# Kernel optimization log

Measured on AMD Instinct MI355X. Metric: run time of the kernel, lower is better.

Reference implementation:

```python
import jax, jax.numpy as jnp
import numpy as np

N_REL = 8


def setup_inputs() -> dict:
    key = jax.random.key(0)
    ks = jax.random.split(key, 16)
    N, E = 100_000, 1_600_000
    rn = lambda k, shape, s=0.1: jax.random.normal(k, shape, dtype=jnp.float32) * s
    return {
        "x": rn(ks[0], (N, 3), 1.0),
        "edge_index": jax.random.randint(ks[1], (2, E), 0, N),
        "edge_attr": rn(ks[2], (E, 2), 1.0),
        "edge_type": jax.random.randint(ks[3], (E,), 0, N_REL),
        "omega": rn(ks[4], (N, 2), 1.0),
        # encoder weights
        "Wn": rn(ks[5], (3, 64)), "bn": jnp.zeros((64,), jnp.float32),
        "We": rn(ks[6], (2, 32)), "be": jnp.zeros((32,), jnp.float32),
        "Wo": rn(ks[7], (2, 64)), "bo": jnp.zeros((64,), jnp.float32),
        # RGCN layer 1 (edge-feature-aware): per-relation W over concat(x_src, e) -> 64
        "W1": rn(ks[8], (N_REL, 96, 64)), "Wroot1": rn(ks[9], (64, 64)), "b1": jnp.zeros((64,), jnp.float32),
        # RGCN layer 2 (PyG RGCNConv, aggr='max')
        "W2": rn(ks[10], (N_REL, 64, 64)), "Wroot2": rn(ks[11], (64, 64)), "b2": jnp.zeros((64,), jnp.float32),
        # head
        "Wagg": rn(ks[12], (128, 64)), "bagg": jnp.zeros((64,), jnp.float32),
        "Wc": rn(ks[13], (64, 1)), "bc": jnp.zeros((1,), jnp.float32),
    }


def reference(x, edge_index, edge_attr, edge_type, omega,
              Wn, bn, We, be, Wo, bo,
              W1, Wroot1, b1, W2, Wroot2, b2,
              Wagg, bagg, Wc, bc):
    N = x.shape[0]
    n = jax.nn.relu(x @ Wn + bn)            # [N,64]
    e = jax.nn.relu(edge_attr @ We + be)    # [E,32]
    o = jax.nn.relu(omega @ Wo + bo)        # [N,64]
    src, dst = edge_index[0], edge_index[1]

    # --- RGCN layer 1: per-relation transform of [x_src || e], sum-aggregate ---
    feat = jnp.concatenate([n[src], e], axis=1)  # [E,96]
    acc = n @ Wroot1 + b1                        # root/self term
    for r in range(N_REL):
        m = (edge_type == r).astype(feat.dtype)[:, None]
        acc = acc + jax.ops.segment_sum((feat * m) @ W1[r], dst, num_segments=N)
    h = jax.nn.relu(acc)                         # [N,64]

    # --- RGCN layer 2: per-relation transform of x_src, max-aggregate per relation, sum over relations ---
    hs = h[src]                                  # [E,64]
    neg = jnp.finfo(h.dtype).min
    acc2 = h @ Wroot2 + b2
    for r in range(N_REL):
        mask = (edge_type == r)[:, None]
        msg = jnp.where(mask, hs @ W2[r], neg)
        mx = jax.ops.segment_max(msg, dst, num_segments=N)
        acc2 = acc2 + jnp.where(mx > neg * 0.5, mx, 0.0)  # empty segments -> 0 (PyG zeros-init scatter)
    h2 = jax.nn.relu(acc2)                       # [N,64]

    out = jax.nn.relu(jnp.concatenate([h2, o], axis=1) @ Wagg + bagg)
    return jnp.tanh(out @ Wc + bc) * 5.0
```

## Files before the change

### kernel.cpp

```cpp
#include <hip/hip_runtime.h>
#include <cmath>

typedef __attribute__((ext_vector_type(8))) short short8;
typedef __attribute__((ext_vector_type(4))) float floatx4;

__device__ __forceinline__ unsigned short rnbf(float f) {
    unsigned u = __float_as_uint(f);
    u += 0x7fffu + ((u >> 16) & 1u);
    return (unsigned short)(u >> 16);
}
__device__ __forceinline__ float bf2f(unsigned short h) {
    return __uint_as_float(((unsigned)h) << 16);
}
__device__ __forceinline__ int rfl(int v) { return __builtin_amdgcn_readfirstlane(v); }
__device__ __forceinline__ float eAct(unsigned ry, float we0, float we1, float bev) {
    float a0 = __uint_as_float(ry & 0xFFFF0000u);
    float a1 = __uint_as_float(ry << 16);
    return fmaxf(fmaf(a1, we1, fmaf(a0, we0, bev)), 0.f);
}
__device__ __forceinline__ unsigned vidx(int x, unsigned pl, int lane) {
    return (((unsigned)x >> 24) & 7u)*pl + (unsigned)(x & 0xFFFFFF)*64u + (unsigned)lane;
}
__device__ __forceinline__ void mstep(int r, float v, int& cur, float& mx, float& add) {
    bool nb = (r != cur);
    add += nb ? mx : 0.f;
    mx = nb ? v : fmaxf(mx, v);
    cur = r;
}

__global__ void k_histd(const int* __restrict__ ei, const int* __restrict__ et,
                        int* __restrict__ deg8, int E)
{
    int e = blockIdx.x*blockDim.x + threadIdx.x;
    if (e < E) atomicAdd(&deg8[ei[E + e]*8 + et[e]], 1);
}
#define SCHUNK 1024
__global__ void k_bsum(const int* __restrict__ deg, int* __restrict__ bsum, int K)
{
    __shared__ int s[256];
    int b = blockIdx.x, t = threadIdx.x;
    int base = b*SCHUNK;
    int v = 0;
    for (int k = t; k < SCHUNK; k += 256) { int i = base + k; v += (i < K) ? deg[i] : 0; }
    s[t] = v; __syncthreads();
    for (int o = 128; o; o >>= 1) { if (t < o) s[t] += s[t+o]; __syncthreads(); }
    if (t == 0) bsum[b] = s[0];
}
__global__ void k_bscan(int* __restrict__ bsum, int nb)
{
    __shared__ int ts[256];
// ... 57 lines not shown
}

#define PB_KEYS 4096
#define PA_CH   4096
#define CNTB    512

__device__ __forceinline__ void dev_cnt(const int* __restrict__ ei,
                                        int* __restrict__ bktCnt,
                                        int E, int nbkt, int cb, int cgrid)
{
    __shared__ int cnt[512];
    for (int j = threadIdx.x; j < nbkt; j += 256) cnt[j] = 0;
    __syncthreads();
    int stride = cgrid*256;
    for (int e = cb*256 + threadIdx.x; e < E; e += stride)
        atomicAdd(&cnt[ei[E + e] >> 9], 1);
    __syncthreads();
    for (int j = threadIdx.x; j < nbkt; j += 256) {
        int c = cnt[j];
        if (c) atomicAdd(&bktCnt[j], c);
    }
}

__device__ __forceinline__ void dev_encV(
    const float* __restrict__ x,
    const float* __restrict__ Wn, const float* __restrict__ bn,
    const unsigned short* __restrict__ wpk, const float* __restrict__ b1,
    float* __restrict__ acc1, unsigned short* __restrict__ Vbf,
    size_t plane, int N, int bid)
{
    int lane = threadIdx.x & 63;
    int wave = threadIdx.x >> 6;
    int n0 = bid*64 + 16*wave;
    int m = lane & 15, q = lane >> 4;
    int node = n0 + m; if (node >= N) node = N - 1;
    float x0 = x[3*node], x1 = x[3*node+1], x2 = x[3*node+2];
    short8 ah[2], al[2];
    #pragma unroll
    for (int ks = 0; ks < 2; ++ks) {
        #pragma unroll
        for (int i = 0; i < 8; ++i) {
            int f = ks*32 + q*8 + i;
            float nf = fmaxf(fmaf(x2, Wn[128+f], fmaf(x1, Wn[64+f], fmaf(x0, Wn[f], bn[f]))), 0.f);
            unsigned short hb = rnbf(nf);
            ah[ks][i] = (short)hb;
            al[ks][i] = (short)rnbf(nf - bf2f(hb));
        }
    }
    {
        floatx4 acc[4];
        #pragma unroll
        for (int jt = 0; jt < 4; ++jt) acc[jt] = (floatx4){0.f,0.f,0.f,0.f};
        #pragma unroll
        for (int ks = 0; ks < 2; ++ks) {
            int unit = 40 + ks;
            #pragma unroll
            for (int jt = 0; jt < 4; ++jt) {
                const unsigned short* qp = wpk + (((size_t)unit*4 + jt)*64 + lane)*16;
                short8 bh = *(const short8*)qp;
                short8 bl = *(const short8*)(qp + 8);
                acc[jt] = __builtin_amdgcn_mfma_f32_16x16x32_bf16(ah[ks], bh, acc[jt], 0,0,0);
                acc[jt] = __builtin_amdgcn_mfma_f32_16x16x32_bf16(ah[ks], bl, acc[jt], 0,0,0);
                acc[jt] = __builtin_amdgcn_mfma_f32_16x16x32_bf16(al[ks], bh, acc[jt], 0,0,0);
            }
        }
        #pragma unroll
        for (int jt = 0; jt < 4; ++jt) {
            float bb = b1[jt*16 + m];
            #pragma unroll
            for (int t = 0; t < 4; ++t) {
                int row = n0 + q*4 + t;
                if (row < N) acc1[(size_t)row*64 + jt*16 + m] = acc[jt][t] + bb;
            }
        }
    }
    for (int p = 0; p < 8; ++p) {
        floatx4 acc[4];
        #pragma unroll
        for (int jt = 0; jt < 4; ++jt) acc[jt] = (floatx4){0.f,0.f,0.f,0.f};
        #pragma unroll
        for (int ks = 0; ks < 2; ++ks) {
            int unit = p*2 + ks;
            #pragma unroll
            for (int jt = 0; jt < 4; ++jt) {
                const unsigned short* qp = wpk + (((size_t)unit*4 + jt)*64 + lane)*16;
                short8 bh = *(const short8*)qp;
                short8 bl = *(const short8*)(qp + 8);
                acc[jt] = __builtin_amdgcn_mfma_f32_16x16x32_bf16(ah[ks], bh, acc[jt], 0,0,0);
                acc[jt] = __builtin_amdgcn_mfma_f32_16x16x32_bf16(ah[ks], bl, acc[jt], 0,0,0);
                acc[jt] = __builtin_amdgcn_mfma_f32_16x16x32_bf16(al[ks], bh, acc[jt], 0,0,0);
            }
        }
        unsigned short* Vp = Vbf + (size_t)p*plane;
        #pragma unroll
        for (int jt = 0; jt < 4; ++jt) {
            #pragma unroll
            for (int t = 0; t < 4; ++t) {
                int row = n0 + q*4 + t;
                if (row < N) Vp[(size_t)row*64 + jt*16 + m] = rnbf(acc[jt][t]);
            }
        }
    }
}

__global__ __launch_bounds__(256) void k_phase1(
    const float* __restrict__ x,
    const float* __restrict__ Wn, const float* __restrict__ bn,
    const unsigned short* __restrict__ wpk, const float* __restrict__ b1,
    float* __restrict__ acc1, unsigned short* __restrict__ Vbf,
    size_t plane, int N,
    const int* __restrict__ ei, int* __restrict__ bktCnt, int E, int nbkt,
    int encBlocks, int cntBlocks)
{
    int bid = (int)blockIdx.x;
    if (bid < encBlocks) {
        dev_encV(x, Wn, bn, wpk, b1, acc1, Vbf, plane, N, bid);
    } else {
        dev_cnt(ei, bktCnt, E, nbkt, bid - encBlocks, cntBlocks);
    }
}

__global__ __launch_bounds__(256) void k_partA(
    const int* __restrict__ ei, const float* __restrict__ ea,
    const int* __restrict__ et, const int* __restrict__ bktCnt,
    int* __restrict__ cursorRel, int2* __restrict__ tmp, int E, int nbkt)
{
    __shared__ int cnt[512], base[512], gbase[256];
    __shared__ int ts[256];
    int t = threadIdx.x;
    {
        int v = (t < nbkt) ? bktCnt[t] : 0;
        ts[t] = v; __syncthreads();
        for (int o = 1; o < 256; o <<= 1) {
            int add = (t >= o) ? ts[t-o] : 0;
            __syncthreads();
            ts[t] += add;
            __syncthreads();
        }
        gbase[t] = ts[t] - v;
// ... 232 lines not shown
            int unit = unitBase + rel*2 + ks;
            #pragma unroll
            for (int jt = 0; jt < 4; ++jt) {
                const unsigned short* qp = wpk + (((size_t)unit*4 + jt)*64 + lane)*16;
                short8 bh = *(const short8*)qp;
                short8 bl = *(const short8*)(qp + 8);
                acc[jt] = __builtin_amdgcn_mfma_f32_16x16x32_bf16(ah[ks], bh, acc[jt], 0,0,0);
                acc[jt] = __builtin_amdgcn_mfma_f32_16x16x32_bf16(ah[ks], bl, acc[jt], 0,0,0);
                acc[jt] = __builtin_amdgcn_mfma_f32_16x16x32_bf16(al[ks], bh, acc[jt], 0,0,0);
            }
        }
        unsigned short* Vp = Vbf + (size_t)p*plane;
        #pragma unroll
        for (int jt = 0; jt < 4; ++jt) {
            #pragma unroll
            for (int t = 0; t < 4; ++t) {
                int row = n0 + q*4 + t;
                if (row < N) Vp[(size_t)row*64 + jt*16 + m] = rnbf(acc[jt][t]);
            }
        }
    }
}

__global__ __launch_bounds__(256) void k_agg1ef(
    const int2* __restrict__ srec, const int* __restrict__ off8,
    const unsigned short* __restrict__ Vbf, size_t plane,
    const float* __restrict__ We, const float* __restrict__ be,
    float* __restrict__ acc1, unsigned short* __restrict__ Sep, int N)
{
    int lane = threadIdx.x & 63;
    int wv = threadIdx.x >> 6;
    unsigned pl = (unsigned)plane;
    float we0 = We[lane & 31], we1 = We[32 + (lane & 31)], bev = be[lane & 31];
    int stride = gridDim.x*4;
    for (int node = blockIdx.x*4 + wv; node < N; node += stride) {
        const int* ofp = off8 + node*8;
        int o0 = rfl(ofp[0]), o8 = rfl(ofp[8]);
        float vsum = 0.f;
        int i = o0;
        for (; i + 16 <= o8; i += 16) {
            int2 q[16];
            #pragma unroll
            for (int u = 0; u < 16; ++u) q[u] = srec[i+u];
            int xs[16];
            #pragma unroll
            for (int u = 0; u < 16; ++u) xs[u] = rfl(q[u].x);
            float v[16];
            #pragma unroll
            for (int u = 0; u < 16; ++u) v[u] = bf2f(Vbf[vidx(xs[u], pl, lane)]);
            float s01 = (v[0]+v[1]) + (v[2]+v[3]);
            float s23 = (v[4]+v[5]) + (v[6]+v[7]);
            float s45 = (v[8]+v[9]) + (v[10]+v[11]);
            float s67 = (v[12]+v[13]) + (v[14]+v[15]);
            vsum += (s01 + s23) + (s45 + s67);
        }
        for (; i + 8 <= o8; i += 8) {
            int2 q0 = srec[i+0], q1 = srec[i+1], q2 = srec[i+2], q3 = srec[i+3];
            int2 q4 = srec[i+4], q5 = srec[i+5], q6 = srec[i+6], q7 = srec[i+7];
            int x0 = rfl(q0.x), x1 = rfl(q1.x), x2 = rfl(q2.x), x3 = rfl(q3.x);
            int x4 = rfl(q4.x), x5 = rfl(q5.x), x6 = rfl(q6.x), x7 = rfl(q7.x);
            float v0 = bf2f(Vbf[vidx(x0, pl, lane)]);
            float v1 = bf2f(Vbf[vidx(x1, pl, lane)]);
            float v2 = bf2f(Vbf[vidx(x2, pl, lane)]);
            float v3 = bf2f(Vbf[vidx(x3, pl, lane)]);
            float v4 = bf2f(Vbf[vidx(x4, pl, lane)]);
            float v5 = bf2f(Vbf[vidx(x5, pl, lane)]);
            float v6 = bf2f(Vbf[vidx(x6, pl, lane)]);
            float v7 = bf2f(Vbf[vidx(x7, pl, lane)]);
            vsum += ((v0+v1)+(v2+v3)) + ((v4+v5)+(v6+v7));
        }
        for (; i < o8; ++i) {
            int xx = rfl(srec[i].x);
            vsum += bf2f(Vbf[vidx(xx, pl, lane)]);
        }
        int o1 = rfl(ofp[1]), o2 = rfl(ofp[2]), o3 = rfl(ofp[3]), o4 = rfl(ofp[4]);
        int o5 = rfl(ofp[5]), o6 = rfl(ofp[6]), o7 = rfl(ofp[7]);
        const unsigned* sy = (const unsigned*)srec;
        float se0=0,se1=0,se2=0,se3=0,se4=0,se5=0,se6=0,se7=0;
        #pragma unroll
        for (int r = 0; r < 8; ++r) {
            int s = (r==0)?o0:(r==1)?o1:(r==2)?o2:(r==3)?o3:(r==4)?o4:(r==5)?o5:(r==6)?o6:o7;
            int e = (r==0)?o1:(r==1)?o2:(r==2)?o3:(r==3)?o4:(r==4)?o5:(r==5)?o6:(r==6)?o7:o8;
            if (s == e) continue;
            float ev = 0.f;
            int k = s;
            for (; k + 4 <= e; k += 4) {
                unsigned y0 = sy[2*(k+0)+1], y1 = sy[2*(k+1)+1];
                unsigned y2 = sy[2*(k+2)+1], y3 = sy[2*(k+3)+1];
                ev += eAct(y0, we0, we1, bev);
                ev += eAct(y1, we0, we1, bev);
                ev += eAct(y2, we0, we1, bev);
                ev += eAct(y3, we0, we1, bev);
            }
            for (; k < e; ++k) ev += eAct(sy[2*k+1], we0, we1, bev);
            if (r == 0) se0 = ev;  if (r == 1) se1 = ev;
            if (r == 2) se2 = ev;  if (r == 3) se3 = ev;
            if (r == 4) se4 = ev;  if (r == 5) se5 = ev;
            if (r == 6) se6 = ev;  if (r == 7) se7 = ev;
        }
        unsigned short* Sp = Sep + (size_t)node*256;
        Sp[0*64 + lane] = rnbf((lane < 32) ? se0 : se1);
        Sp[1*64 + lane] = rnbf((lane < 32) ? se2 : se3);
        Sp[2*64 + lane] = rnbf((lane < 32) ? se4 : se5);
        Sp[3*64 + lane] = rnbf((lane < 32) ? se6 : se7);
        if (o0 != o8) acc1[(size_t)node*64 + lane] += vsum;
    }
}

__global__ __launch_bounds__(256) void k_agg1e(
    const int2* __restrict__ srec, const int* __restrict__ off8,
    const unsigned short* __restrict__ Vbf, size_t plane,
    const float* __restrict__ We, const float* __restrict__ be,
    float* __restrict__ acc1, unsigned short* __restrict__ Sep, int N, int Gc)
{
    int lane = threadIdx.x & 63;
    int wv = threadIdx.x >> 6;
    float we0 = We[lane & 31], we1 = We[32 + (lane & 31)], bev = be[lane & 31];
    int stride = gridDim.x*4;
    for (int node = blockIdx.x*4 + wv; node < N; node += stride) {
        int o0 = rfl(off8[node*8+0]), o1 = rfl(off8[node*8+1]), o2 = rfl(off8[node*8+2]);
        int o3 = rfl(off8[node*8+3]), o4 = rfl(off8[node*8+4]), o5 = rfl(off8[node*8+5]);
        int o6 = rfl(off8[node*8+6]), o7 = rfl(off8[node*8+7]), o8 = rfl(off8[node*8+8]);
        float vsum = 0.f;
        float se0=0,se1=0,se2=0,se3=0,se4=0,se5=0,se6=0,se7=0;
        #pragma unroll
        for (int r = 0; r < 8; ++r) {
            int s = (r==0)?o0:(r==1)?o1:(r==2)?o2:(r==3)?o3:(r==4)?o4:(r==5)?o5:(r==6)?o6:o7;
            int e = (r==0)?o1:(r==1)?o2:(r==2)?o3:(r==3)?o4:(r==4)?o5:(r==5)?o6:(r==6)?o7:o8;
// ... 23 lines not shown
                ev += eAct((unsigned)q4.y, we0, we1, bev);
                ev += eAct((unsigned)q5.y, we0, we1, bev);
                ev += eAct((unsigned)q6.y, we0, we1, bev);
                ev += eAct((unsigned)q7.y, we0, we1, bev);
            }
            for (; i < e; ++i) {
                int2 qq = srec[i];
                if (doV) vsum += bf2f(Vp[(size_t)(rfl(qq.x) & 0xFFFFFF)*64 + lane]);
                ev += eAct((unsigned)qq.y, we0, we1, bev);
            }
            if (r == 0) se0 = ev;  if (r == 1) se1 = ev;
            if (r == 2) se2 = ev;  if (r == 3) se3 = ev;
            if (r == 4) se4 = ev;  if (r == 5) se5 = ev;
            if (r == 6) se6 = ev;  if (r == 7) se7 = ev;
        }
        unsigned short* Sp = Sep + (size_t)node*256;
        Sp[0*64 + lane] = rnbf((lane < 32) ? se0 : se1);
        Sp[1*64 + lane] = rnbf((lane < 32) ? se2 : se3);
        Sp[2*64 + lane] = rnbf((lane < 32) ? se4 : se5);
        Sp[3*64 + lane] = rnbf((lane < 32) ? se6 : se7);
        if (o0 != o8) acc1[(size_t)node*64 + lane] += vsum;
    }
}

__global__ __launch_bounds__(256) void k_agg1v(
    const int2* __restrict__ srec, const int* __restrict__ off8,
    const unsigned short* __restrict__ Vbf, size_t plane,
    float* __restrict__ acc1, int N, int g0, int g1)
{
    int lane = threadIdx.x & 63;
    int wv = threadIdx.x >> 6;
    int stride = gridDim.x*4;
    for (int node = blockIdx.x*4 + wv; node < N; node += stride) {
        float vsum = 0.f;
        bool any = false;
        for (int r = g0; r < g1; ++r) {
            int s = rfl(off8[node*8 + r]);
            int e = rfl(off8[node*8 + r + 1]);
            if (s == e) continue;
            any = true;
            const unsigned short* Vp = Vbf + (size_t)(r - g0)*plane;
            int i = s;
            for (; i + 8 <= e; i += 8) {
                int s0 = rfl(srec[i+0].x) & 0xFFFFFF, s1 = rfl(srec[i+1].x) & 0xFFFFFF;
                int s2 = rfl(srec[i+2].x) & 0xFFFFFF, s3 = rfl(srec[i+3].x) & 0xFFFFFF;
                int s4 = rfl(srec[i+4].x) & 0xFFFFFF, s5 = rfl(srec[i+5].x) & 0xFFFFFF;
                int s6 = rfl(srec[i+6].x) & 0xFFFFFF, s7 = rfl(srec[i+7].x) & 0xFFFFFF;
                float v0 = bf2f(Vp[(size_t)s0*64 + lane]), v1 = bf2f(Vp[(size_t)s1*64 + lane]);
                float v2 = bf2f(Vp[(size_t)s2*64 + lane]), v3 = bf2f(Vp[(size_t)s3*64 + lane]);
                float v4 = bf2f(Vp[(size_t)s4*64 + lane]), v5 = bf2f(Vp[(size_t)s5*64 + lane]);
                float v6 = bf2f(Vp[(size_t)s6*64 + lane]), v7 = bf2f(Vp[(size_t)s7*64 + lane]);
                vsum += ((v0+v1)+(v2+v3)) + ((v4+v5)+(v6+v7));
            }
            for (; i < e; ++i) {
                int sx = rfl(srec[i].x) & 0xFFFFFF;
                vsum += bf2f(Vp[(size_t)sx*64 + lane]);
            }
        }
        if (any) acc1[(size_t)node*64 + lane] += vsum;
    }
}

__global__ __launch_bounds__(256) void k_segemm(
    const unsigned short* __restrict__ Sep, const unsigned short* __restrict__ wpk,
    float* __restrict__ acc1, int N)
{
    int lane = threadIdx.x & 63;
    int wave = threadIdx.x >> 6;
    int n0 = blockIdx.x*64 + 16*wave;
    int m = lane & 15, q = lane >> 4;
    int node = n0 + m;
    if (node >= N) node = N - 1;
    floatx4 acc[4];
    #pragma unroll
    for (int jt = 0; jt < 4; ++jt) acc[jt] = (floatx4){0.f,0.f,0.f,0.f};
    for (int rel = 0; rel < 8; ++rel) {
        short8 ah = *(const short8*)(Sep + (size_t)node*256 + rel*32 + q*8);
        int unit = 32 + rel;
        #pragma unroll
        for (int jt = 0; jt < 4; ++jt) {
            const unsigned short* qp = wpk + (((size_t)unit*4 + jt)*64 + lane)*16;
            short8 bh = *(const short8*)qp;
            short8 bl = *(const short8*)(qp + 8);
            acc[jt] = __builtin_amdgcn_mfma_f32_16x16x32_bf16(ah, bh, acc[jt], 0,0,0);
            acc[jt] = __builtin_amdgcn_mfma_f32_16x16x32_bf16(ah, bl, acc[jt], 0,0,0);
        }
    }
    #pragma unroll
    for (int jt = 0; jt < 4; ++jt) {
        #pragma unroll
        for (int t = 0; t < 4; ++t) {
            int row = n0 + q*4 + t;
            if (row < N) acc1[(size_t)row*64 + jt*16 + m] += acc[jt][t];
        }
    }
}

__global__ __launch_bounds__(256) void k_hrowB(
    float* __restrict__ acc1, float* __restrict__ acc2,
    const unsigned short* __restrict__ wpk, const float* __restrict__ b2, int N)
{
    int lane = threadIdx.x & 63;
    int wave = threadIdx.x >> 6;
    int n0 = blockIdx.x*64 + 16*wave;
    int m = lane & 15, q = lane >> 4;
    int node = n0 + m;
    if (node >= N) node = N - 1;
    float4* Fr = (float4*)(acc1 + (size_t)node*64);
    short8 ah[2], al[2];
    #pragma unroll
    for (int ks = 0; ks < 2; ++ks) {
        float4 u0 = Fr[ks*8 + q*2];
        float4 u1 = Fr[ks*8 + q*2 + 1];
        float fv[8] = {u0.x,u0.y,u0.z,u0.w,u1.x,u1.y,u1.z,u1.w};
        #pragma unroll
        for (int i = 0; i < 8; ++i) {
            float hv = fmaxf(fv[i], 0.f);
            fv[i] = hv;
            unsigned short hb = rnbf(hv);
            ah[ks][i] = (short)hb;
// ... 5 lines not shown
    floatx4 acc[4];
    #pragma unroll
    for (int jt = 0; jt < 4; ++jt) acc[jt] = (floatx4){0.f,0.f,0.f,0.f};
    #pragma unroll
    for (int ks = 0; ks < 2; ++ks) {
        int unit = 42 + ks;
        #pragma unroll
        for (int jt = 0; jt < 4; ++jt) {
            const unsigned short* qp = wpk + (((size_t)unit*4 + jt)*64 + lane)*16;
            short8 bh = *(const short8*)qp;
            short8 bl = *(const short8*)(qp + 8);
            acc[jt] = __builtin_amdgcn_mfma_f32_16x16x32_bf16(ah[ks], bh, acc[jt], 0,0,0);
            acc[jt] = __builtin_amdgcn_mfma_f32_16x16x32_bf16(ah[ks], bl, acc[jt], 0,0,0);
            acc[jt] = __builtin_amdgcn_mfma_f32_16x16x32_bf16(al[ks], bh, acc[jt], 0,0,0);
        }
    }
    #pragma unroll
    for (int jt = 0; jt < 4; ++jt) {
        float bb = b2[jt*16 + m];
        #pragma unroll
        for (int t = 0; t < 4; ++t) {
            int row = n0 + q*4 + t;
            if (row < N) acc2[(size_t)row*64 + jt*16 + m] = acc[jt][t] + bb;
        }
    }
}

__global__ __launch_bounds__(256) void k_seghrowV(
    const unsigned short* __restrict__ Sep, const unsigned short* __restrict__ wpk,
    const float* __restrict__ acc1, float* __restrict__ acc2,
    const float* __restrict__ b2, unsigned short* __restrict__ Vbf,
    size_t plane, int N)
{
    __shared__ __align__(16) float sS[4][16][68];
    int lane = threadIdx.x & 63;
    int wave = threadIdx.x >> 6;
    int n0 = blockIdx.x*64 + 16*wave;
    int m = lane & 15, q = lane >> 4;
    int node = n0 + m;
    if (node >= N) node = N - 1;
    {
        floatx4 sacc[4];
        #pragma unroll
        for (int jt = 0; jt < 4; ++jt) sacc[jt] = (floatx4){0.f,0.f,0.f,0.f};
        for (int rel = 0; rel < 8; ++rel) {
            short8 sa = *(const short8*)(Sep + (size_t)node*256 + rel*32 + q*8);
            int unit = 32 + rel;
            #pragma unroll
            for (int jt = 0; jt < 4; ++jt) {
                const unsigned short* qp = wpk + (((size_t)unit*4 + jt)*64 + lane)*16;
                short8 bh = *(const short8*)qp;
                short8 bl = *(const short8*)(qp + 8);
                sacc[jt] = __builtin_amdgcn_mfma_f32_16x16x32_bf16(sa, bh, sacc[jt], 0,0,0);
                sacc[jt] = __builtin_amdgcn_mfma_f32_16x16x32_bf16(sa, bl, sacc[jt], 0,0,0);
            }
        }
        #pragma unroll
        for (int jt = 0; jt < 4; ++jt) {
            #pragma unroll
            for (int t = 0; t < 4; ++t)
                sS[wave][q*4 + t][jt*16 + m] = sacc[jt][t];
        }
    }
    __syncthreads();
    const float4* Fr = (const float4*)(acc1 + (size_t)node*64);
    short8 ah[2], al[2];
    #pragma unroll
    for (int ks = 0; ks < 2; ++ks) {
        float4 u0 = Fr[ks*8 + q*2];
        float4 u1 = Fr[ks*8 + q*2 + 1];
        float fv[8] = {u0.x,u0.y,u0.z,u0.w,u1.x,u1.y,u1.z,u1.w};
        #pragma unroll
        for (int i = 0; i < 8; ++i) {
            float hv = fmaxf(fv[i] + sS[wave][m][ks*32 + q*8 + i], 0.f);
            unsigned short hb = rnbf(hv);
            ah[ks][i] = (short)hb;
            al[ks][i] = (short)rnbf(hv - bf2f(hb));
        }
    }
    {
        floatx4 acc[4];
        #pragma unroll
        for (int jt = 0; jt < 4; ++jt) acc[jt] = (floatx4){0.f,0.f,0.f,0.f};
        #pragma unroll
        for (int ks = 0; ks < 2; ++ks) {
            int unit = 42 + ks;
            #pragma unroll
            for (int jt = 0; jt < 4; ++jt) {
                const unsigned short* qp = wpk + (((size_t)unit*4 + jt)*64 + lane)*16;
                short8 bh = *(const short8*)qp;
                short8 bl = *(const short8*)(qp + 8);
                acc[jt] = __builtin_amdgcn_mfma_f32_16x16x32_bf16(ah[ks], bh, acc[jt], 0,0,0);
                acc[jt] = __builtin_amdgcn_mfma_f32_16x16x32_bf16(ah[ks], bl, acc[jt], 0,0,0);
                acc[jt] = __builtin_amdgcn_mfma_f32_16x16x32_bf16(al[ks], bh, acc[jt], 0,0,0);
            }
        }
        #pragma unroll
        for (int jt = 0; jt < 4; ++jt) {
            float bb = b2[jt*16 + m];
            #pragma unroll
            for (int t = 0; t < 4; ++t) {
                int row = n0 + q*4 + t;
                if (row < N) acc2[(size_t)row*64 + jt*16 + m] = acc[jt][t] + bb;
            }
        }
    }
    for (int p = 0; p < 8; ++p) {
        floatx4 acc[4];
        #pragma unroll
        for (int jt = 0; jt < 4; ++jt) acc[jt] = (floatx4){0.f,0.f,0.f,0.f};
        #pragma unroll
        for (int ks = 0; ks < 2; ++ks) {
            int unit = 16 + p*2 + ks;
            #pragma unroll
            for (int jt = 0; jt < 4; ++jt) {
                const unsigned short* qp = wpk + (((size_t)unit*4 + jt)*64 + lane)*16;
                short8 bh = *(const short8*)qp;
                short8 bl = *(const short8*)(qp + 8);
                acc[jt] = __builtin_amdgcn_mfma_f32_16x16x32_bf16(ah[ks], bh, acc[jt], 0,0,0);
                acc[jt] = __builtin_amdgcn_mfma_f32_16x16x32_bf16(ah[ks], bl, acc[jt], 0,0,0);
                acc[jt] = __builtin_amdgcn_mfma_f32_16x16x32_bf16(al[ks], bh, acc[jt], 0,0,0);
            }
        }
        unsigned short* Vp = Vbf + (size_t)p*plane;
        #pragma unroll
        for (int jt = 0; jt < 4; ++jt) {
            #pragma unroll
            for (int t = 0; t < 4; ++t) {
                int row = n0 + q*4 + t;
                if (row < N) Vp[(size_t)row*64 + jt*16 + m] = rnbf(acc[jt][t]);
            }
        }
    }
}

__global__ __launch_bounds__(256) void k_agg2f(
    const int2* __restrict__ srec, const int* __restrict__ off8,
    const unsigned short* __restrict__ Ubf, size_t plane,
    float* __restrict__ acc2, int N)
{
    int lane = threadIdx.x & 63;
    int wv = threadIdx.x >> 6;
    unsigned pl = (unsigned)plane;
    int stride = gridDim.x*4;
    for (int node = blockIdx.x*4 + wv; node < N; node += stride) {
        int o0 = rfl(off8[node*8]);
        int o8 = rfl(off8[node*8 + 8]);
        if (o0 == o8) continue;
        float add = 0.f, mx = 0.f;
        int cur = -1;
        int i = o0;
        for (; i + 16 <= o8; i += 16) {
            int2 q[16];
            #pragma unroll
// ... 190 lines not shown
    int nb = (K8 + SCHUNK - 1)/SCHUNK;

    #define ALIGN256(p) ((char*)(((size_t)(p) + 255) & ~(size_t)255))
    char* pp = (char*)d_ws;
    float* nbuf   = (float*)pp;  pp = ALIGN256(pp + (size_t)N*64*4);
    float* acc1   = (float*)pp;  pp = ALIGN256(pp + (size_t)N*64*4);
    int2*  srec   = (int2*)pp;   pp = ALIGN256(pp + (size_t)E*8);
    int*   deg8   = (int*)pp;    pp = ALIGN256(pp + (size_t)K8*4);
    int*   off8   = (int*)pp;    pp = ALIGN256(pp + (size_t)(K8+1)*4);
    int*   cursor = (int*)pp;    pp = ALIGN256(pp + (size_t)K8*4);
    int*   bsum   = (int*)pp;    pp = ALIGN256(pp + (size_t)nb*4);
    unsigned short* wpk = (unsigned short*)pp;
    pp = ALIGN256(pp + (size_t)48*4*64*16*2);
    unsigned short* Sepool = (unsigned short*)pp;
    pp = ALIGN256(pp + (size_t)N*256*2);
    size_t off = (size_t)(pp - (char*)d_ws);
    size_t planeElems = (size_t)N*64;
    size_t avail = (ws_size > off) ? (ws_size - off) : 0;
    int G = (int)(avail / (planeElems*2));
    if (G > 8) G = 8;
    if (G < 1) G = 1;
    unsigned short* Vbf = (unsigned short*)pp;
    float* acc2 = nbuf;

    int gblocks = (N + 63)/64;
    int nbkt = (N + 511) >> 9;
    bool fastSort = (N <= 131072) && ((size_t)E*8 <= (size_t)N*256*2);
    int* bktCnt = deg8;
    int* cursorRel = deg8 + 512;

    if (fastSort) hipMemsetAsync(deg8, 0, 4096, stream);
    else          hipMemsetAsync(deg8, 0, (size_t)K8*4, stream);
    k_wpack<<<192, 64, 0, stream>>>(W1, W2, Wroot1, Wroot2, Wagg, wpk);

    if (G == 8 && fastSort) {
        k_phase1<<<gblocks + CNTB, 256, 0, stream>>>(x, Wn, bn, wpk, b1, acc1, Vbf,
                                                     planeElems, N, ei, bktCnt, E, nbkt,
                                                     gblocks, CNTB);
    } else if (G == 8) {
        k_phase1<<<gblocks, 256, 0, stream>>>(x, Wn, bn, wpk, b1, acc1, Vbf,
                                              planeElems, N, ei, bktCnt, E, nbkt,
                                              gblocks, 0);
    } else {
        k_encB<<<gblocks, 256, 0, stream>>>(x, Wn, bn, wpk, b1, nbuf, acc1, N);
        if (fastSort)
            k_phase1<<<CNTB, 256, 0, stream>>>(x, Wn, bn, wpk, b1, acc1, Vbf,
                                               planeElems, N, ei, bktCnt, E, nbkt,
                                               0, CNTB);
    }

    if (fastSort) {
        int2* tmp = (int2*)Sepool;
        k_partA<<<(E + PA_CH - 1)/PA_CH, 256, 0, stream>>>(ei, ea, et, bktCnt,
                                                           cursorRel, tmp, E, nbkt);
        k_partB2<<<nbkt, 256, 0, stream>>>(tmp, bktCnt, off8, srec, K8, nbkt);
    } else {
        k_histd<<<(E + 255)/256, 256, 0, stream>>>(ei, et, deg8, E);
        k_bsum<<<nb, 256, 0, stream>>>(deg8, bsum, K8);
        k_bscan<<<1, 256, 0, stream>>>(bsum, nb);
        k_bapply<<<nb, 256, 0, stream>>>(deg8, bsum, off8, cursor, K8);
        k_scatd<<<(E + 255)/256, 256, 0, stream>>>(ei, ea, et, cursor, srec, E);
    }

    int aggBlocks = 4096;
    if (G == 8) {
        k_agg1ef<<<aggBlocks, 256, 0, stream>>>(srec, off8, Vbf, planeElems, We, be,
                                                acc1, Sepool, N);
        k_seghrowV<<<gblocks, 256, 0, stream>>>(Sepool, wpk, acc1, acc2, b2,
                                                Vbf, planeElems, N);
        k_agg2f<<<aggBlocks, 256, 0, stream>>>(srec, off8, Vbf, planeElems, acc2, N);
    } else {
        int Gc1 = G;
        k_vgemmB<<<gblocks, 256, 0, stream>>>(nbuf, wpk, 0, 0, Gc1, Vbf, planeElems, N);
        k_agg1e<<<aggBlocks, 256, 0, stream>>>(srec, off8, Vbf, planeElems, We, be,
                                               acc1, Sepool, N, Gc1);
        for (int g0 = Gc1; g0 < 8; g0 += G) {
            int Gc = (8 - g0 < G) ? (8 - g0) : G;
            k_vgemmB<<<gblocks, 256, 0, stream>>>(nbuf, wpk, 0, g0, Gc, Vbf, planeElems, N);
            k_agg1v<<<aggBlocks, 256, 0, stream>>>(srec, off8, Vbf, planeElems,
                                                   acc1, N, g0, g0 + Gc);
        }
        k_segemm<<<gblocks, 256, 0, stream>>>(Sepool, wpk, acc1, N);
        k_hrowB<<<gblocks, 256, 0, stream>>>(acc1, acc2, wpk, b2, N);
        for (int g0 = 0; g0 < 8; g0 += G) {
            int Gc = (8 - g0 < G) ? (8 - g0) : G;
            k_vgemmB<<<gblocks, 256, 0, stream>>>(acc1, wpk, 16, g0, Gc, Vbf, planeElems, N);
            k_agg2<<<aggBlocks, 256, 0, stream>>>(srec, off8, Vbf, planeElems,
                                                  acc2, N, g0, g0 + Gc);
        }
    }
    k_finB<<<gblocks, 256, 0, stream>>>(acc2, omega, Wo, bo, wpk, bagg, Wc, bc, out, N);
}
// ... 1 lines not shown
```

Baseline: 452.3 us.

## Aggregate raw node features per relation before applying layer-1 weights

Layer 1 no longer precomputes eight per-relation transformed planes and gathers from them per edge. Each node's neighbours' bf16 encoded features now go into eight per-relation sums, using a single compact gather table. A new MFMA kernel then applies the W1 relation weights and the edge-feature weights to those sums. This shrinks the random-gather working set so more of it stays in cache, at the cost of writing and re-reading a [N,512] bf16 intermediate, extra select arithmetic per edge, and coarser bf16 rounding of the per-relation sums.

```diff
diff --git a/kernel.cpp b/kernel.cpp
--- a/kernel.cpp
+++ b/kernel.cpp
@@ -26,6 +26,13 @@
     add += nb ? mx : 0.f;
     mx = nb ? v : fmaxf(mx, v);
     cur = r;
+}
+__device__ __forceinline__ void acc8(int r, float v,
+    float& a0, float& a1, float& a2, float& a3,
+    float& a4, float& a5, float& a6, float& a7)
+{
+    a0 += (r==0)?v:0.f; a1 += (r==1)?v:0.f; a2 += (r==2)?v:0.f; a3 += (r==3)?v:0.f;
+    a4 += (r==4)?v:0.f; a5 += (r==5)?v:0.f; a6 += (r==6)?v:0.f; a7 += (r==7)?v:0.f;
 }
 
 __global__ void k_histd(const int* __restrict__ ei, const int* __restrict__ et,
@@ -129,17 +136,26 @@
     }
 }
 
-__device__ __forceinline__ void dev_encV(
+__device__ __forceinline__ void dev_enc(
     const float* __restrict__ x,
     const float* __restrict__ Wn, const float* __restrict__ bn,
     const unsigned short* __restrict__ wpk, const float* __restrict__ b1,
-    float* __restrict__ acc1, unsigned short* __restrict__ Vbf,
-    size_t plane, int N, int bid)
+    float* __restrict__ acc1, unsigned short* __restrict__ nb16,
+    int N, int bid)
 {
     int lane = threadIdx.x & 63;
     int wave = threadIdx.x >> 6;
     int n0 = bid*64 + 16*wave;
     int m = lane & 15, q = lane >> 4;
+    #pragma unroll 4
+    for (int t = 0; t < 16; ++t) {
+        int nd = n0 + t;
+        if (nd < N) {
+            float x0 = x[3*nd], x1 = x[3*nd+1], x2 = x[3*nd+2];
+            float nj = fmaxf(fmaf(x2, Wn[128+lane], fmaf(x1, Wn[64+lane], fmaf(x0, Wn[lane], bn[lane]))), 0.f);
+            nb16[(size_t)nd*64 + lane] = rnbf(nj);
+        }
+    }
     int node = n0 + m; if (node >= N) node = N - 1;
     float x0 = x[3*node], x1 = x[3*node+1], x2 = x[3*node+2];
     short8 ah[2], al[2];
@@ -154,58 +170,29 @@
             al[ks][i] = (short)rnbf(nf - bf2f(hb));
         }
     }
-    {
-        floatx4 acc[4];
-        #pragma unroll
-        for (int jt = 0; jt < 4; ++jt) acc[jt] = (floatx4){0.f,0.f,0.f,0.f};
-        #pragma unroll
-        for (int ks = 0; ks < 2; ++ks) {
-            int unit = 40 + ks;
-            #pragma unroll
-            for (int jt = 0; jt < 4; ++jt) {
-                const unsigned short* qp = wpk + (((size_t)unit*4 + jt)*64 + lane)*16;
-                short8 bh = *(const short8*)qp;
-                short8 bl = *(const short8*)(qp + 8);
-                acc[jt] = __builtin_amdgcn_mfma_f32_16x16x32_bf16(ah[ks], bh, acc[jt], 0,0,0);
-                acc[jt] = __builtin_amdgcn_mfma_f32_16x16x32_bf16(ah[ks], bl, acc[jt], 0,0,0);
-                acc[jt] = __builtin_amdgcn_mfma_f32_16x16x32_bf16(al[ks], bh, acc[jt], 0,0,0);
-            }
-        }
+    floatx4 acc[4];
+    #pragma unroll
+    for (int jt = 0; jt < 4; ++jt) acc[jt] = (floatx4){0.f,0.f,0.f,0.f};
+    #pragma unroll
+    for (int ks = 0; ks < 2; ++ks) {
+        int unit = 40 + ks;
         #pragma unroll
         for (int jt = 0; jt < 4; ++jt) {
-            float bb = b1[jt*16 + m];
-            #pragma unroll
-            for (int t = 0; t < 4; ++t) {
-                int row = n0 + q*4 + t;
-                if (row < N) acc1[(size_t)row*64 + jt*16 + m] = acc[jt][t] + bb;
-            }
-        }
-    }
-    for (int p = 0; p < 8; ++p) {
-        floatx4 acc[4];
-        #pragma unroll
-        for (int jt = 0; jt < 4; ++jt) acc[jt] = (floatx4){0.f,0.f,0.f,0.f};
-        #pragma unroll
-        for (int ks = 0; ks < 2; ++ks) {
-            int unit = p*2 + ks;
-            #pragma unroll
-            for (int jt = 0; jt < 4; ++jt) {
-                const unsigned short* qp = wpk + (((size_t)unit*4 + jt)*64 + lane)*16;
-                short8 bh = *(const short8*)qp;
-                short8 bl = *(const short8*)(qp + 8);
-                acc[jt] = __builtin_amdgcn_mfma_f32_16x16x32_bf16(ah[ks], bh, acc[jt], 0,0,0);
-                acc[jt] = __builtin_amdgcn_mfma_f32_16x16x32_bf16(ah[ks], bl, acc[jt], 0,0,0);
-                acc[jt] = __builtin_amdgcn_mfma_f32_16x16x32_bf16(al[ks], bh, acc[jt], 0,0,0);
-            }
-        }
-        unsigned short* Vp = Vbf + (size_t)p*plane;
-        #pragma unroll
-        for (int jt = 0; jt < 4; ++jt) {
-            #pragma unroll
-            for (int t = 0; t < 4; ++t) {
-                int row = n0 + q*4 + t;
-                if (row < N) Vp[(size_t)row*64 + jt*16 + m] = rnbf(acc[jt][t]);
-            }
+            const unsigned short* qp = wpk + (((size_t)unit*4 + jt)*64 + lane)*16;
+            short8 bh = *(const short8*)qp;
+            short8 bl = *(const short8*)(qp + 8);
+            acc[jt] = __builtin_amdgcn_mfma_f32_16x16x32_bf16(ah[ks], bh, acc[jt], 0,0,0);
+            acc[jt] = __builtin_amdgcn_mfma_f32_16x16x32_bf16(ah[ks], bl, acc[jt], 0,0,0);
+            acc[jt] = __builtin_amdgcn_mfma_f32_16x16x32_bf16(al[ks], bh, acc[jt], 0,0,0);
+        }
+    }
+    #pragma unroll
+    for (int jt = 0; jt < 4; ++jt) {
+        float bb = b1[jt*16 + m];
+        #pragma unroll
+        for (int t = 0; t < 4; ++t) {
+            int row = n0 + q*4 + t;
+            if (row < N) acc1[(size_t)row*64 + jt*16 + m] = acc[jt][t] + bb;
         }
     }
 }
@@ -214,14 +201,13 @@
     const float* __restrict__ x,
     const float* __restrict__ Wn, const float* __restrict__ bn,
     const unsigned short* __restrict__ wpk, const float* __restrict__ b1,
-    float* __restrict__ acc1, unsigned short* __restrict__ Vbf,
-    size_t plane, int N,
+    float* __restrict__ acc1, unsigned short* __restrict__ nb16, int N,
     const int* __restrict__ ei, int* __restrict__ bktCnt, int E, int nbkt,
     int encBlocks, int cntBlocks)
 {
     int bid = (int)blockIdx.x;
     if (bid < encBlocks) {
-        dev_encV(x, Wn, bn, wpk, b1, acc1, Vbf, plane, N, bid);
+        dev_enc(x, Wn, bn, wpk, b1, acc1, nb16, N, bid);
     } else {
         dev_cnt(ei, bktCnt, E, nbkt, bid - encBlocks, cntBlocks);
     }
@@ -500,21 +486,20 @@
     }
 }
 
-__global__ __launch_bounds__(256) void k_agg1ef(
+__global__ __launch_bounds__(256) void k_agg1n(
     const int2* __restrict__ srec, const int* __restrict__ off8,
-    const unsigned short* __restrict__ Vbf, size_t plane,
+    const unsigned short* __restrict__ nb16,
     const float* __restrict__ We, const float* __restrict__ be,
-    float* __restrict__ acc1, unsigned short* __restrict__ Sep, int N)
+    unsigned short* __restrict__ nsum, unsigned short* __restrict__ Sep, int N)
 {
     int lane = threadIdx.x & 63;
     int wv = threadIdx.x >> 6;
-    unsigned pl = (unsigned)plane;
     float we0 = We[lane & 31], we1 = We[32 + (lane & 31)], bev = be[lane & 31];
     int stride = gridDim.x*4;
     for (int node = blockIdx.x*4 + wv; node < N; node += stride) {
         const int* ofp = off8 + node*8;
         int o0 = rfl(ofp[0]), o8 = rfl(ofp[8]);
-        float vsum = 0.f;
+        float ns0=0,ns1=0,ns2=0,ns3=0,ns4=0,ns5=0,ns6=0,ns7=0;
         int i = o0;
         for (; i + 16 <= o8; i += 16) {
             int2 q[16];
@@ -525,31 +510,39 @@
             for (int u = 0; u < 16; ++u) xs[u] = rfl(q[u].x);
             float v[16];
             #pragma unroll
-            for (int u = 0; u < 16; ++u) v[u] = bf2f(Vbf[vidx(xs[u], pl, lane)]);
-            float s01 = (v[0]+v[1]) + (v[2]+v[3]);
-            float s23 = (v[4]+v[5]) + (v[6]+v[7]);
-            float s45 = (v[8]+v[9]) + (v[10]+v[11]);
-            float s67 = (v[12]+v[13]) + (v[14]+v[15]);
-            vsum += (s01 + s23) + (s45 + s67);
+            for (int u = 0; u < 16; ++u)
+                v[u] = bf2f(nb16[(unsigned)(xs[u] & 0xFFFFFF)*64u + (unsigned)lane]);
+            #pragma unroll
+            for (int u = 0; u < 16; ++u)
+                acc8((int)(((unsigned)xs[u] >> 24) & 7u), v[u],
+                     ns0,ns1,ns2,ns3,ns4,ns5,ns6,ns7);
         }
         for (; i + 8 <= o8; i += 8) {
             int2 q0 = srec[i+0], q1 = srec[i+1], q2 = srec[i+2], q3 = srec[i+3];
             int2 q4 = srec[i+4], q5 = srec[i+5], q6 = srec[i+6], q7 = srec[i+7];
             int x0 = rfl(q0.x), x1 = rfl(q1.x), x2 = rfl(q2.x), x3 = rfl(q3.x);
             int x4 = rfl(q4.x), x5 = rfl(q5.x), x6 = rfl(q6.x), x7 = rfl(q7.x);
-            float v0 = bf2f(Vbf[vidx(x0, pl, lane)]);
-            float v1 = bf2f(Vbf[vidx(x1, pl, lane)]);
-            float v2 = bf2f(Vbf[vidx(x2, pl, lane)]);
-            float v3 = bf2f(Vbf[vidx(x3, pl, lane)]);
-            float v4 = bf2f(Vbf[vidx(x4, pl, lane)]);
-            float v5 = bf2f(Vbf[vidx(x5, pl, lane)]);
-            float v6 = bf2f(Vbf[vidx(x6, pl, lane)]);
-            float v7 = bf2f(Vbf[vidx(x7, pl, lane)]);
-            vsum += ((v0+v1)+(v2+v3)) + ((v4+v5)+(v6+v7));
+            float v0 = bf2f(nb16[(unsigned)(x0 & 0xFFFFFF)*64u + (unsigned)lane]);
+            float v1 = bf2f(nb16[(unsigned)(x1 & 0xFFFFFF)*64u + (unsigned)lane]);
+            float v2 = bf2f(nb16[(unsigned)(x2 & 0xFFFFFF)*64u + (unsigned)lane]);
+            float v3 = bf2f(nb16[(unsigned)(x3 & 0xFFFFFF)*64u + (unsigned)lane]);
+            float v4 = bf2f(nb16[(unsigned)(x4 & 0xFFFFFF)*64u + (unsigned)lane]);
+            float v5 = bf2f(nb16[(unsigned)(x5 & 0xFFFFFF)*64u + (unsigned)lane]);
+            float v6 = bf2f(nb16[(unsigned)(x6 & 0xFFFFFF)*64u + (unsigned)lane]);
+            float v7 = bf2f(nb16[(unsigned)(x7 & 0xFFFFFF)*64u + (unsigned)lane]);
+            acc8((int)(((unsigned)x0 >> 24) & 7u), v0, ns0,ns1,ns2,ns3,ns4,ns5,ns6,ns7);
+            acc8((int)(((unsigned)x1 >> 24) & 7u), v1, ns0,ns1,ns2,ns3,ns4,ns5,ns6,ns7);
+            acc8((int)(((unsigned)x2 >> 24) & 7u), v2, ns0,ns1,ns2,ns3,ns4,ns5,ns6,ns7);
+            acc8((int)(((unsigned)x3 >> 24) & 7u), v3, ns0,ns1,ns2,ns3,ns4,ns5,ns6,ns7);
+            acc8((int)(((unsigned)x4 >> 24) & 7u), v4, ns0,ns1,ns2,ns3,ns4,ns5,ns6,ns7);
+            acc8((int)(((unsigned)x5 >> 24) & 7u), v5, ns0,ns1,ns2,ns3,ns4,ns5,ns6,ns7);
+            acc8((int)(((unsigned)x6 >> 24) & 7u), v6, ns0,ns1,ns2,ns3,ns4,ns5,ns6,ns7);
+            acc8((int)(((unsigned)x7 >> 24) & 7u), v7, ns0,ns1,ns2,ns3,ns4,ns5,ns6,ns7);
         }
         for (; i < o8; ++i) {
             int xx = rfl(srec[i].x);
-            vsum += bf2f(Vbf[vidx(xx, pl, lane)]);
+            float v = bf2f(nb16[(unsigned)(xx & 0xFFFFFF)*64u + (unsigned)lane]);
+            acc8((int)(((unsigned)xx >> 24) & 7u), v, ns0,ns1,ns2,ns3,ns4,ns5,ns6,ns7);
         }
         int o1 = rfl(ofp[1]), o2 = rfl(ofp[2]), o3 = rfl(ofp[3]), o4 = rfl(ofp[4]);
         int o5 = rfl(ofp[5]), o6 = rfl(ofp[6]), o7 = rfl(ofp[7]);
@@ -576,12 +569,150 @@
             if (r == 4) se4 = ev;  if (r == 5) se5 = ev;
             if (r == 6) se6 = ev;  if (r == 7) se7 = ev;
         }
+        unsigned short* np = nsum + (size_t)node*512;
+        np[0*64 + lane] = rnbf(ns0);
+        np[1*64 + lane] = rnbf(ns1);
+        np[2*64 + lane] = rnbf(ns2);
+        np[3*64 + lane] = rnbf(ns3);
+        np[4*64 + lane] = rnbf(ns4);
+        np[5*64 + lane] = rnbf(ns5);
+        np[6*64 + lane] = rnbf(ns6);
+        np[7*64 + lane] = rnbf(ns7);
         unsigned short* Sp = Sep + (size_t)node*256;
         Sp[0*64 + lane] = rnbf((lane < 32) ? se0 : se1);
         Sp[1*64 + lane] = rnbf((lane < 32) ? se2 : se3);
         Sp[2*64 + lane] = rnbf((lane < 32) ? se4 : se5);
         Sp[3*64 + lane] = rnbf((lane < 32) ? se6 : se7);
-        if (o0 != o8) acc1[(size_t)node*64 + lane] += vsum;
+    }
+}
+
+__global__ __launch_bounds__(256) void k_gemm1(
+    const unsigned short* __restrict__ nsum, const unsigned short* __restrict__ Sep,
+    const unsigned short* __restrict__ wpk, float* __restrict__ acc1, int N)
+{
+    int lane = threadIdx.x & 63;
+    int wave = threadIdx.x >> 6;
+    int n0 = blockIdx.x*64 + 16*wave;
+    int m = lane & 15, q = lane >> 4;
+    int node = n0 + m;
+    if (node >= N) node = N - 1;
+    floatx4 acc[4];
+    #pragma unroll
+    for (int jt = 0; jt < 4; ++jt) acc[jt] = (floatx4){0.f,0.f,0.f,0.f};
+    for (int rel = 0; rel < 8; ++rel) {
+        #pragma unroll
+        for (int ks = 0; ks < 2; ++ks) {
+            short8 na = *(const short8*)(nsum + (size_t)node*512 + rel*64 + ks*32 + q*8);
+            int unit = rel*2 + ks;
+            #pragma unroll
+            for (int jt = 0; jt < 4; ++jt) {
+                const unsigned short* qp = wpk + (((size_t)unit*4 + jt)*64 + lane)*16;
+                short8 bh = *(const short8*)qp;
+                short8 bl = *(const short8*)(qp + 8);
+                acc[jt] = __builtin_amdgcn_mfma_f32_16x16x32_bf16(na, bh, acc[jt], 0,0,0);
+                acc[jt] = __builtin_amdgcn_mfma_f32_16x16x32_bf16(na, bl, acc[jt], 0,0,0);
+            }
+        }
+        short8 sa = *(const short8*)(Sep + (size_t)node*256 + rel*32 + q*8);
+        int unit2 = 32 + rel;
+        #pragma unroll
+        for (int jt = 0; jt < 4; ++jt) {
+            const unsigned short* qp = wpk + (((size_t)unit2*4 + jt)*64 + lane)*16;
+            short8 bh = *(const short8*)qp;
+            short8 bl = *(const short8*)(qp + 8);
+            acc[jt] = __builtin_amdgcn_mfma_f32_16x16x32_bf16(sa, bh, acc[jt], 0,0,0);
+            acc[jt] = __builtin_amdgcn_mfma_f32_16x16x32_bf16(sa, bl, acc[jt], 0,0,0);
+        }
+    }
+    #pragma unroll
+    for (int jt = 0; jt < 4; ++jt) {
+        #pragma unroll
+        for (int t = 0; t < 4; ++t) {
+            int row = n0 + q*4 + t;
+            if (row < N) acc1[(size_t)row*64 + jt*16 + m] += acc[jt][t];
+        }
+    }
+}
+
+__global__ __launch_bounds__(256) void k_hrowV(
+    const float* __restrict__ acc1, float* __restrict__ acc2,
+    const unsigned short* __restrict__ wpk, const float* __restrict__ b2,
+    unsigned short* __restrict__ Vbf, size_t plane, int N)
+{
+    int lane = threadIdx.x & 63;
+    int wave = threadIdx.x >> 6;
+    int n0 = blockIdx.x*64 + 16*wave;
+    int m = lane & 15, q = lane >> 4;
+    int node = n0 + m;
+    if (node >= N) node = N - 1;
+    const float4* Fr = (const float4*)(acc1 + (size_t)node*64);
+    short8 ah[2], al[2];
+    #pragma unroll
+    for (int ks = 0; ks < 2; ++ks) {
+        float4 u0 = Fr[ks*8 + q*2];
+        float4 u1 = Fr[ks*8 + q*2 + 1];
+        float fv[8] = {u0.x,u0.y,u0.z,u0.w,u1.x,u1.y,u1.z,u1.w};
+        #pragma unroll
+        for (int i = 0; i < 8; ++i) {
+            float hv = fmaxf(fv[i], 0.f);
+            unsigned short hb = rnbf(hv);
+            ah[ks][i] = (short)hb;
+            al[ks][i] = (short)rnbf(hv - bf2f(hb));
+        }
+    }
+    {
+        floatx4 acc[4];
+        #pragma unroll
+        for (int jt = 0; jt < 4; ++jt) acc[jt] = (floatx4){0.f,0.f,0.f,0.f};
+        #pragma unroll
+        for (int ks = 0; ks < 2; ++ks) {
+            int unit = 42 + ks;
+            #pragma unroll
+            for (int jt = 0; jt < 4; ++jt) {
+                const unsigned short* qp = wpk + (((size_t)unit*4 + jt)*64 + lane)*16;
+                short8 bh = *(const short8*)qp;
+                short8 bl = *(const short8*)(qp + 8);
+                acc[jt] = __builtin_amdgcn_mfma_f32_16x16x32_bf16(ah[ks], bh, acc[jt], 0,0,0);
+                acc[jt] = __builtin_amdgcn_mfma_f32_16x16x32_bf16(ah[ks], bl, acc[jt], 0,0,0);
+                acc[jt] = __builtin_amdgcn_mfma_f32_16x16x32_bf16(al[ks], bh, acc[jt], 0,0,0);
+            }
+        }
+        #pragma unroll
+        for (int jt = 0; jt < 4; ++jt) {
+            float bb = b2[jt*16 + m];
+            #pragma unroll
+            for (int t = 0; t < 4; ++t) {
+                int row = n0 + q*4 + t;
+                if (row < N) acc2[(size_t)row*64 + jt*16 + m] = acc[jt][t] + bb;
+            }
+        }
+    }
+    for (int p = 0; p < 8; ++p) {
+        floatx4 acc[4];
+        #pragma unroll
+        for (int jt = 0; jt < 4; ++jt) acc[jt] = (floatx4){0.f,0.f,0.f,0.f};
+        #pragma unroll
+        for (int ks = 0; ks < 2; ++ks) {
+            int unit = 16 + p*2 + ks;
+            #pragma unroll
+            for (int jt = 0; jt < 4; ++jt) {
+                const unsigned short* qp = wpk + (((size_t)unit*4 + jt)*64 + lane)*16;
+                short8 bh = *(const short8*)qp;
+                short8 bl = *(const short8*)(qp + 8);
+                acc[jt] = __builtin_amdgcn_mfma_f32_16x16x32_bf16(ah[ks], bh, acc[jt], 0,0,0);
+                acc[jt] = __builtin_amdgcn_mfma_f32_16x16x32_bf16(ah[ks], bl, acc[jt], 0,0,0);
+                acc[jt] = __builtin_amdgcn_mfma_f32_16x16x32_bf16(al[ks], bh, acc[jt], 0,0,0);
+            }
+        }
+        unsigned short* Vp = Vbf + (size_t)p*plane;
+        #pragma unroll
+        for (int jt = 0; jt < 4; ++jt) {
+            #pragma unroll
+            for (int t = 0; t < 4; ++t) {
+                int row = n0 + q*4 + t;
+                if (row < N) Vp[(size_t)row*64 + jt*16 + m] = rnbf(acc[jt][t]);
+            }
+        }
     }
 }
 
@@ -651,7 +782,6 @@
         if (o0 != o8) acc1[(size_t)node*64 + lane] += vsum;
     }
 }
-
 __global__ __launch_bounds__(256) void k_agg1v(
     const int2* __restrict__ srec, const int* __restrict__ off8,
     const unsigned short* __restrict__ Vbf, size_t plane,
@@ -689,7 +819,6 @@
         if (any) acc1[(size_t)node*64 + lane] += vsum;
     }
 }
-
 __global__ __launch_bounds__(256) void k_segemm(
     const unsigned short* __restrict__ Sep, const unsigned short* __restrict__ wpk,
     float* __restrict__ acc1, int N)
@@ -724,7 +853,6 @@
         }
     }
 }
-
 __global__ __launch_bounds__(256) void k_hrowB(
     float* __restrict__ acc1, float* __restrict__ acc2,
     const unsigned short* __restrict__ wpk, const float* __restrict__ b2, int N)
@@ -776,114 +904,6 @@
         for (int t = 0; t < 4; ++t) {
             int row = n0 + q*4 + t;
             if (row < N) acc2[(size_t)row*64 + jt*16 + m] = acc[jt][t] + bb;
-        }
-    }
-}
-
-__global__ __launch_bounds__(256) void k_seghrowV(
-    const unsigned short* __restrict__ Sep, const unsigned short* __restrict__ wpk,
-    const float* __restrict__ acc1, float* __restrict__ acc2,
-    const float* __restrict__ b2, unsigned short* __restrict__ Vbf,
-    size_t plane, int N)
-{
-    __shared__ __align__(16) float sS[4][16][68];
-    int lane = threadIdx.x & 63;
-    int wave = threadIdx.x >> 6;
-    int n0 = blockIdx.x*64 + 16*wave;
-    int m = lane & 15, q = lane >> 4;
-    int node = n0 + m;
-    if (node >= N) node = N - 1;
-    {
-        floatx4 sacc[4];
-        #pragma unroll
-        for (int jt = 0; jt < 4; ++jt) sacc[jt] = (floatx4){0.f,0.f,0.f,0.f};
-        for (int rel = 0; rel < 8; ++rel) {
-            short8 sa = *(const short8*)(Sep + (size_t)node*256 + rel*32 + q*8);
-            int unit = 32 + rel;
-            #pragma unroll
-            for (int jt = 0; jt < 4; ++jt) {
-                const unsigned short* qp = wpk + (((size_t)unit*4 + jt)*64 + lane)*16;
-                short8 bh = *(const short8*)qp;
-                short8 bl = *(const short8*)(qp + 8);
-                sacc[jt] = __builtin_amdgcn_mfma_f32_16x16x32_bf16(sa, bh, sacc[jt], 0,0,0);
-                sacc[jt] = __builtin_amdgcn_mfma_f32_16x16x32_bf16(sa, bl, sacc[jt], 0,0,0);
-            }
-        }
-        #pragma unroll
-        for (int jt = 0; jt < 4; ++jt) {
-            #pragma unroll
-            for (int t = 0; t < 4; ++t)
-                sS[wave][q*4 + t][jt*16 + m] = sacc[jt][t];
-        }
-    }
-    __syncthreads();
-    const float4* Fr = (const float4*)(acc1 + (size_t)node*64);
-    short8 ah[2], al[2];
-    #pragma unroll
-    for (int ks = 0; ks < 2; ++ks) {
-        float4 u0 = Fr[ks*8 + q*2];
-        float4 u1 = Fr[ks*8 + q*2 + 1];
-        float fv[8] = {u0.x,u0.y,u0.z,u0.w,u1.x,u1.y,u1.z,u1.w};
-        #pragma unroll
-        for (int i = 0; i < 8; ++i) {
-            float hv = fmaxf(fv[i] + sS[wave][m][ks*32 + q*8 + i], 0.f);
-            unsigned short hb = rnbf(hv);
-            ah[ks][i] = (short)hb;
-            al[ks][i] = (short)rnbf(hv - bf2f(hb));
-        }
-    }
-    {
-        floatx4 acc[4];
-        #pragma unroll
-        for (int jt = 0; jt < 4; ++jt) acc[jt] = (floatx4){0.f,0.f,0.f,0.f};
-        #pragma unroll
-        for (int ks = 0; ks < 2; ++ks) {
-            int unit = 42 + ks;
-            #pragma unroll
-            for (int jt = 0; jt < 4; ++jt) {
-                const unsigned short* qp = wpk + (((size_t)unit*4 + jt)*64 + lane)*16;
-                short8 bh = *(const short8*)qp;
-                short8 bl = *(const short8*)(qp + 8);
-                acc[jt] = __builtin_amdgcn_mfma_f32_16x16x32_bf16(ah[ks], bh, acc[jt], 0,0,0);
-                acc[jt] = __builtin_amdgcn_mfma_f32_16x16x32_bf16(ah[ks], bl, acc[jt], 0,0,0);
-                acc[jt] = __builtin_amdgcn_mfma_f32_16x16x32_bf16(al[ks], bh, acc[jt], 0,0,0);
-            }
-        }
-        #pragma unroll
-        for (int jt = 0; jt < 4; ++jt) {
-            float bb = b2[jt*16 + m];
-            #pragma unroll
-            for (int t = 0; t < 4; ++t) {
-                int row = n0 + q*4 + t;
-                if (row < N) acc2[(size_t)row*64 + jt*16 + m] = acc[jt][t] + bb;
-            }
-        }
-    }
-    for (int p = 0; p < 8; ++p) {
-        floatx4 acc[4];
-        #pragma unroll
-        for (int jt = 0; jt < 4; ++jt) acc[jt] = (floatx4){0.f,0.f,0.f,0.f};
-        #pragma unroll
-        for (int ks = 0; ks < 2; ++ks) {
-            int unit = 16 + p*2 + ks;
-            #pragma unroll
-            for (int jt = 0; jt < 4; ++jt) {
-                const unsigned short* qp = wpk + (((size_t)unit*4 + jt)*64 + lane)*16;
-                short8 bh = *(const short8*)qp;
-                short8 bl = *(const short8*)(qp + 8);
-                acc[jt] = __builtin_amdgcn_mfma_f32_16x16x32_bf16(ah[ks], bh, acc[jt], 0,0,0);
-                acc[jt] = __builtin_amdgcn_mfma_f32_16x16x32_bf16(ah[ks], bl, acc[jt], 0,0,0);
-                acc[jt] = __builtin_amdgcn_mfma_f32_16x16x32_bf16(al[ks], bh, acc[jt], 0,0,0);
-            }
-        }
-        unsigned short* Vp = Vbf + (size_t)p*plane;
-        #pragma unroll
-        for (int jt = 0; jt < 4; ++jt) {
-            #pragma unroll
-            for (int t = 0; t < 4; ++t) {
-                int row = n0 + q*4 + t;
-                if (row < N) Vp[(size_t)row*64 + jt*16 + m] = rnbf(acc[jt][t]);
-            }
         }
     }
 }
@@ -1120,6 +1140,7 @@
     if (G < 1) G = 1;
     unsigned short* Vbf = (unsigned short*)pp;
     float* acc2 = nbuf;
+    unsigned short* nb16 = (unsigned short*)nbuf;
 
     int gblocks = (N + 63)/64;
     int nbkt = (N + 511) >> 9;
@@ -1131,20 +1152,15 @@
     else          hipMemsetAsync(deg8, 0, (size_t)K8*4, stream);
     k_wpack<<<192, 64, 0, stream>>>(W1, W2, Wroot1, Wroot2, Wagg, wpk);
 
-    if (G == 8 && fastSort) {
-        k_phase1<<<gblocks + CNTB, 256, 0, stream>>>(x, Wn, bn, wpk, b1, acc1, Vbf,
-                                                     planeElems, N, ei, bktCnt, E, nbkt,
-                                                     gblocks, CNTB);
-    } else if (G == 8) {
-        k_phase1<<<gblocks, 256, 0, stream>>>(x, Wn, bn, wpk, b1, acc1, Vbf,
-                                              planeElems, N, ei, bktCnt, E, nbkt,
-                                              gblocks, 0);
+    if (G == 8) {
+        int cb = fastSort ? CNTB : 0;
+        k_phase1<<<gblocks + cb, 256, 0, stream>>>(x, Wn, bn, wpk, b1, acc1, nb16, N,
+                                                   ei, bktCnt, E, nbkt, gblocks, cb);
     } else {
         k_encB<<<gblocks, 256, 0, stream>>>(x, Wn, bn, wpk, b1, nbuf, acc1, N);
         if (fastSort)
-            k_phase1<<<CNTB, 256, 0, stream>>>(x, Wn, bn, wpk, b1, acc1, Vbf,
-                                               planeElems, N, ei, bktCnt, E, nbkt,
-                                               0, CNTB);
+            k_phase1<<<CNTB, 256, 0, stream>>>(x, Wn, bn, wpk, b1, acc1, nb16, N,
+                                               ei, bktCnt, E, nbkt, 0, CNTB);
     }
 
     if (fastSort) {
@@ -1162,10 +1178,10 @@
 
     int aggBlocks = 4096;
     if (G == 8) {
-        k_agg1ef<<<aggBlocks, 256, 0, stream>>>(srec, off8, Vbf, planeElems, We, be,
-                                                acc1, Sepool, N);
-        k_seghrowV<<<gblocks, 256, 0, stream>>>(Sepool, wpk, acc1, acc2, b2,
-                                                Vbf, planeElems, N);
+        k_agg1n<<<aggBlocks, 256, 0, stream>>>(srec, off8, nb16, We, be,
+                                               Vbf, Sepool, N);
+        k_gemm1<<<gblocks, 256, 0, stream>>>(Vbf, Sepool, wpk, acc1, N);
+        k_hrowV<<<gblocks, 256, 0, stream>>>(acc1, acc2, wpk, b2, Vbf, planeElems, N);
         k_agg2f<<<aggBlocks, 256, 0, stream>>>(srec, off8, Vbf, planeElems, acc2, N);
     } else {
         int Gc1 = G;
```

New measurement: 512.0 us. +13.2%, slower.
